# Kernel tuning notes

Measured on AMD Instinct MI355X. Metric: run time of the kernel, lower is better.

The kernel has to match this reference:

```python
import jax, jax.numpy as jnp
import numpy as np

DIM = 1024
NUM_HEADS = 16
HEAD_DIM = DIM // NUM_HEADS
MLP_DIM = 4 * DIM
EPS = 1e-5


def layer_norm(x, g, b):
    mu = jnp.mean(x, axis=-1, keepdims=True)
    var = jnp.mean(jnp.square(x - mu), axis=-1, keepdims=True)
    return (x - mu) * jax.lax.rsqrt(var + EPS) * g + b


def setup_inputs() -> dict:
    key = jax.random.key(0)
    ks = jax.random.split(key, 12)
    B, L = 2, 2048
    s = lambda n: 1.0 / np.sqrt(n)
    return {
        "x": jax.random.normal(ks[0], (B, L, DIM), jnp.float32),
        "attn_mask": jnp.tril(jnp.ones((L, L), jnp.int32))[None, None],  # [1,1,L,L]
        "w_qkv": jax.random.normal(ks[1], (DIM, 3 * DIM), jnp.float32) * s(DIM),
        "b_qkv": jnp.zeros((3 * DIM,), jnp.float32),
        "w_proj": jax.random.normal(ks[2], (DIM, DIM), jnp.float32) * s(DIM),
        "b_proj": jnp.zeros((DIM,), jnp.float32),
        "w_fc1": jax.random.normal(ks[3], (DIM, MLP_DIM), jnp.float32) * s(DIM),
        "b_fc1": jnp.zeros((MLP_DIM,), jnp.float32),
        "w_fc2": jax.random.normal(ks[4], (MLP_DIM, DIM), jnp.float32) * s(MLP_DIM),
        "b_fc2": jnp.zeros((DIM,), jnp.float32),
        "g1": jnp.ones((DIM,), jnp.float32),
        "beta1": jnp.zeros((DIM,), jnp.float32),
        "g2": jnp.ones((DIM,), jnp.float32),
        "beta2": jnp.zeros((DIM,), jnp.float32),
    }


def reference(x, attn_mask, w_qkv, b_qkv, w_proj, b_proj, w_fc1, b_fc1,
              w_fc2, b_fc2, g1, beta1, g2, beta2):
    B, L, D = x.shape
    scale = HEAD_DIM ** -0.5

    # --- attention branch (pre-norm) ---
    h = layer_norm(x, g1, beta1)
    qkv = h @ w_qkv + b_qkv                                  # [B,L,3D]
    qkv = qkv.reshape(B, L, 3, NUM_HEADS, HEAD_DIM)
    q = qkv[:, :, 0].transpose(0, 2, 1, 3)                   # [B,H,L,hd]
    k = qkv[:, :, 1].transpose(0, 2, 1, 3)
    v = qkv[:, :, 2].transpose(0, 2, 1, 3)
    attn = jnp.einsum('bhqd,bhkd->bhqk', q, k) * scale       # [B,H,L,L]
    attn = jnp.where(attn_mask == 0, -jnp.inf, attn)
    attn = jax.nn.softmax(attn, axis=-1)
    y = jnp.einsum('bhqk,bhkd->bhqd', attn, v)               # [B,H,L,hd]
    y = y.transpose(0, 2, 1, 3).reshape(B, L, D)
    y = y @ w_proj + b_proj
    x = x + y

    # --- MLP branch (pre-norm) ---
    h = layer_norm(x, g2, beta2)
    h = jax.nn.gelu(h @ w_fc1 + b_fc1, approximate=False)
    h = h @ w_fc2 + b_fc2
    return x + h
```

## Files before the change

### kernel.cpp

```cpp
#include <hip/hip_runtime.h>
#include <hip/hip_bf16.h>
#include <stdint.h>

typedef unsigned short u16;
typedef __attribute__((ext_vector_type(8))) short bf16x8;
typedef __attribute__((ext_vector_type(4))) float f32x4;
typedef __attribute__((ext_vector_type(4))) unsigned short u16x4;

#define DEVI static __device__ __forceinline__

DEVI u16 f2bf(float f) {
    unsigned int u = __builtin_bit_cast(unsigned int, f);
    return (u16)((u + 0x7fffu + ((u >> 16) & 1u)) >> 16);
}

DEVI float gelu_f(float v) {
    const float z = 1.5957691216f * (v + 0.044715f * v * v * v);
    return v / (1.0f + __expf(-z));
}

DEVI void async_copy16(const void* g, void* l) {
    __builtin_amdgcn_global_load_lds((const __attribute__((address_space(1))) void*)g,
                                     (__attribute__((address_space(3))) void*)l,
                                     16, 0, 0);
}

__global__ __launch_bounds__(256) void tcvt_kernel(const float* __restrict__ src,
                                                   u16* __restrict__ dst,
                                                   int K, int N) {
    __shared__ float tile[32][33];
    const int k0 = blockIdx.x * 32, n0 = blockIdx.y * 32;
    const int t = threadIdx.x;
    const int c = t & 31, r0 = t >> 5;
#pragma unroll
    for (int p = 0; p < 4; ++p) {
        const int r = r0 + p * 8;
        tile[r][c] = src[(size_t)(k0 + r) * N + n0 + c];
    }
    __syncthreads();
#pragma unroll
    for (int p = 0; p < 4; ++p) {
        const int r = r0 + p * 8;
        dst[(size_t)(n0 + r) * K + k0 + c] = f2bf(tile[c][r]);
    }
}

__global__ __launch_bounds__(256) void ln_kernel(const float* __restrict__ x,
                                                 const float* __restrict__ gw,
                                                 const float* __restrict__ bw,
                                                 u16* __restrict__ out) {
    const int row = blockIdx.x;
    const int t = threadIdx.x;
    const float4 v = ((const float4*)(x + (size_t)row * 1024))[t];
    float s  = v.x + v.y + v.z + v.w;
    float ss = v.x * v.x + v.y * v.y + v.z * v.z + v.w * v.w;
#pragma unroll
    for (int off = 32; off > 0; off >>= 1) {
        s  += __shfl_down(s, off);
        ss += __shfl_down(ss, off);
    }
    __shared__ float red[8];
    const int wv = t >> 6;
    if ((t & 63) == 0) { red[wv] = s; red[4 + wv] = ss; }
    __syncthreads();
    if (t == 0) {
        red[0] = red[0] + red[1] + red[2] + red[3];
        red[4] = red[4] + red[5] + red[6] + red[7];
    }
    __syncthreads();
    const float mean = red[0] * (1.0f / 1024.0f);
    const float var  = red[4] * (1.0f / 1024.0f) - mean * mean;
    const float rstd = rsqrtf(var + 1e-5f);
    const float4 gv = ((const float4*)gw)[t];
    const float4 bv = ((const float4*)bw)[t];
    u16x4 o;
    o[0] = f2bf((v.x - mean) * rstd * gv.x + bv.x);
    o[1] = f2bf((v.y - mean) * rstd * gv.y + bv.y);
    o[2] = f2bf((v.z - mean) * rstd * gv.z + bv.z);
    o[3] = f2bf((v.w - mean) * rstd * gv.w + bv.w);
    ((u16x4*)out)[(size_t)row * 256 + t] = o;
}

DEVI void stage64(const char* g, size_t ldb, char* lds0, int lane, int wv) {
    const int colsw = ((lane & 3) << 4) ^ (lane & 32);
    const int rl = lane >> 2;
#pragma unroll
    for (int i = 0; i < 4; ++i) {
        const int s = wv * 4 + i;
        const int kh = s >> 3, c = s & 7;
        async_copy16(g + (size_t)(c * 16 + rl) * ldb + kh * 64 + colsw,
                     lds0 + s * 1024);
    }
}

template <int EPI, int SPLITK>
__global__ __launch_bounds__(256, 4) void gemmv6(const u16* __restrict__ A,
                                                 const u16* __restrict__ Bt,
                                                 const float* __restrict__ bias,
                                                 void* __restrict__ out0,
                                                 void* __restrict__ out1,
                                                 void* __restrict__ out2,
                                                 int M, int N, int K) {
    __shared__ __align__(16) char As[16384];
    __shared__ __align__(16) char Bs[16384];
    const int tid = threadIdx.x;
    const int lane = tid & 63, wv = tid >> 6;
    const int wr = wv >> 1, wc = wv & 1;
    const int g = lane >> 4, qq = lane & 15;
    const int rdoff = qq * 64 + ((g * 16) ^ ((qq & 8) << 2));

    const int nwg = gridDim.x;
    int id = blockIdx.x;
    id = (id & 7) * (nwg >> 3) + (id >> 3);
    const int MT = M >> 7, NTn = N >> 7;
    const int slice = id / (MT * NTn);
    const int r2 = id % (MT * NTn);
    const int m0 = (r2 % MT) << 7;
    const int n0 = (r2 / MT) << 7;
    const int Ks = K / SPLITK;
    const int NT = Ks >> 6;
    const size_t ldb = (size_t)K * 2;

    const char* pa = (const char*)A + (size_t)m0 * ldb + (size_t)slice * Ks * 2;
    const char* pb = (const char*)Bt + (size_t)n0 * ldb + (size_t)slice * Ks * 2;

    f32x4 acc[4][4] = {};

    for (int t = 0; t < NT; ++t) {
        stage64(pa + (size_t)t * 128, ldb, As, lane, wv);
        stage64(pb + (size_t)t * 128, ldb, Bs, lane, wv);
        __syncthreads();
#pragma unroll
        for (int kh = 0; kh < 2; ++kh) {
            bf16x8 fa[4], fb[4];
#pragma unroll
            for (int fn = 0; fn < 4; ++fn)
                fb[fn] = *(const bf16x8*)(Bs + (kh * 8 + wc * 4 + fn) * 1024 + rdoff);
#pragma unroll
            for (int fm = 0; fm < 4; ++fm)
                fa[fm] = *(const bf16x8*)(As + (kh * 8 + wr * 4 + fm) * 1024 + rdoff);
#pragma unroll
            for (int fm = 0; fm < 4; ++fm)
#pragma unroll
                for (int fn = 0; fn < 4; ++fn)
                    acc[fm][fn] = __builtin_amdgcn_mfma_f32_16x16x32_bf16(fa[fm], fb[fn],
                                                                          acc[fm][fn], 0, 0, 0);
        }
        __syncthreads();
    }

#pragma unroll
    for (int fm = 0; fm < 4; ++fm) {
#pragma unroll
        for (int fn = 0; fn < 4; ++fn) {
            const int mrow = m0 + wr * 64 + fm * 16 + g * 4;
            const int ncol = n0 + wc * 64 + fn * 16 + qq;
            if constexpr (EPI == 0) {
                const float bs = bias[ncol];
                const int sec = ncol >> 10;
                const int hd_ = ncol & 1023;
                const int hh = hd_ >> 6, dd = hd_ & 63;
                if (sec == 2) {
                    const int b_ = mrow >> 11, l_ = mrow & 2047;
                    u16x4 pk;
#pragma unroll
                    for (int r = 0; r < 4; ++r) pk[r] = f2bf(acc[fm][fn][r] + bs);
                    *(u16x4*)((u16*)out2 + ((size_t)((b_ * 16 + hh) * 64 + dd)) * 2048 + l_) = pk;
                } else {
                    u16* dst = (sec == 0) ? (u16*)out0 : (u16*)out1;
                    const float sc = (sec == 0) ? 0.125f : 1.0f;
#pragma unroll
                    for (int r = 0; r < 4; ++r) {
                        const int mr = mrow + r;
                        const int b_ = mr >> 11, l_ = mr & 2047;
                        dst[((size_t)((b_ * 16 + hh) * 2048 + l_)) * 64 + dd] =
                            f2bf((acc[fm][fn][r] + bs) * sc);
                    }
                }
            } else if constexpr (EPI == 2) {
                const float bs = bias[ncol];
                u16* dst = (u16*)out0;
#pragma unroll
                for (int r = 0; r < 4; ++r)
                    dst[(size_t)(mrow + r) * N + ncol] = f2bf(gelu_f(acc[fm][fn][r] + bs));
            } else {
                float* dst = (float*)out0 + (size_t)slice * M * N;
#pragma unroll
                for (int r = 0; r < 4; ++r)
                    dst[(size_t)(mrow + r) * N + ncol] = acc[fm][fn][r];
            }
        }
    }
}

template <int SPLIT>
__global__ __launch_bounds__(256) void reduceN_kernel(const float* __restrict__ p,
                                                      const float* __restrict__ bias,
                                                      const float* __restrict__ res,
                                                      float* __restrict__ out,
                                                      int MN4, int N4) {
    const int i = blockIdx.x * 256 + threadIdx.x;
    float4 s = ((const float4*)p)[i];
#pragma unroll
    for (int s2 = 1; s2 < SPLIT; ++s2) {
        const float4 q = ((const float4*)p)[(size_t)s2 * MN4 + i];
        s.x += q.x; s.y += q.y; s.z += q.z; s.w += q.w;
    }
    const float4 r = ((const float4*)res)[i];
    const float4 bs = ((const float4*)bias)[i & (N4 - 1)];
    float4 o;
    o.x = s.x + r.x + bs.x;
    o.y = s.y + r.y + bs.y;
    o.z = s.z + r.z + bs.z;
    o.w = s.w + r.w + bs.w;
    ((float4*)out)[i] = o;
}

DEVI void stage_kv(const char* kbase, const char* vbase, int key0,
                   u16* ksm, u16* vsm, int wv, int lane) {
#pragma unroll
    for (int i = 0; i < 2; ++i) {
        const int c = wv + i * 4;
        const int off = c * 1024 + lane * 16;
        const int row = off >> 7;
        const int scol = (off & 127) ^ ((row & 7) << 4);
        async_copy16(kbase + (size_t)key0 * 128 + (size_t)row * 128 + scol,
                     (char*)ksm + c * 1024);
    }
#pragma unroll
    for (int i = 0; i < 2; ++i) {
        const int c = wv + i * 4;
        const int row = c * 8 + (lane >> 3);
        const int scol = ((lane & 7) * 16) ^ ((row & 7) << 4);
        async_copy16(vbase + (size_t)row * 4096 + (size_t)key0 * 2 + scol,
                     (char*)vsm + c * 1024);
    }
}

__global__ __launch_bounds__(256, 3) void attn_kernel(const u16* __restrict__ Q,
                                                      const u16* __restrict__ Kk,
                                                      const u16* __restrict__ Vt,
                                                      u16* __restrict__ Y) {
    const int bh = blockIdx.y;
    const int b_ = bh >> 4, hh = bh & 15;
    const int qb = gridDim.x - 1 - blockIdx.x;
    const int tid = threadIdx.x;
    const int wv = tid >> 6, lane = tid & 63;
    const int g = lane >> 4, qi = lane & 15;
    const int xsw = (qi & 7) << 4;
    const int q0 = qb * 64 + wv * 16;
    const int qg = q0 + qi;

    __shared__ __align__(16) u16 Ksm[2][4096];
    __shared__ __align__(16) u16 Vsm[2][4096];
    __shared__ __align__(16) u16 Pl[4][16][72];

    const u16*  Qb = Q + ((size_t)bh * 2048 + q0) * 64;
    const char* Kb = (const char*)(Kk + (size_t)bh * 2048 * 64);
    const char* Vb = (const char*)(Vt + (size_t)bh * 64 * 2048);

    bf16x8 qf[2];
#pragma unroll
    for (int ks = 0; ks < 2; ++ks)
        qf[ks] = *(const bf16x8*)(Qb + qi * 64 + ks * 32 + g * 8);

    f32x4 oacc[4] = {};
    float m_run = -1e30f, l_run = 0.0f;
    const int ntile = qb + 1;

    stage_kv(Kb, Vb, 0, Ksm[0], Vsm[0], wv, lane);
    __syncthreads();

    int cur = 0;
    for (int kt = 0; kt < ntile; ++kt) {
        const int key0 = kt * 64;
        if (kt + 1 < ntile)
            stage_kv(Kb, Vb, key0 + 64, Ksm[cur ^ 1], Vsm[cur ^ 1], wv, lane);

        f32x4 sacc[4] = {};
#pragma unroll
        for (int ks = 0; ks < 2; ++ks) {
#pragma unroll
            for (int kc = 0; kc < 4; ++kc) {
                const int rk = kc * 16 + qi;
                const bf16x8 ak = *(const bf16x8*)((const char*)Ksm[cur] + rk * 128 +
                                                   ((ks * 64 + g * 16) ^ xsw));
                sacc[kc] = __builtin_amdgcn_mfma_f32_16x16x32_bf16(ak, qf[ks], sacc[kc], 0, 0, 0);
            }
        }

        float p[4][4];
        float mymax = -1e30f;
        if (kt == ntile - 1) {
#pragma unroll
            for (int kc = 0; kc < 4; ++kc) {
#pragma unroll
                for (int r = 0; r < 4; ++r) {
                    const int key = key0 + kc * 16 + g * 4 + r;
                    float sv = sacc[kc][r];
                    if (key > qg) sv = -__builtin_inff();
                    p[kc][r] = sv;
                    mymax = fmaxf(mymax, sv);
                }
            }
        } else {
#pragma unroll
            for (int kc = 0; kc < 4; ++kc) {
#pragma unroll
                for (int r = 0; r < 4; ++r) {
                    p[kc][r] = sacc[kc][r];
                    mymax = fmaxf(mymax, sacc[kc][r]);
                }
            }
        }
        mymax = fmaxf(mymax, __shfl_xor(mymax, 16));
        mymax = fmaxf(mymax, __shfl_xor(mymax, 32));
        const float m_new = fmaxf(m_run, mymax);
        const float alpha = __expf(m_run - m_new);
        float lsum = 0.0f;
#pragma unroll
        for (int kc = 0; kc < 4; ++kc) {
#pragma unroll
            for (int r = 0; r < 4; ++r) {
                const float e = __expf(p[kc][r] - m_new);
                p[kc][r] = e;
                lsum += e;
            }
        }
        lsum += __shfl_xor(lsum, 16);
        lsum += __shfl_xor(lsum, 32);
        l_run = l_run * alpha + lsum;
        m_run = m_new;
#pragma unroll
        for (int c = 0; c < 4; ++c) {
#pragma unroll
            for (int r = 0; r < 4; ++r) oacc[c][r] *= alpha;
        }
#pragma unroll
        for (int kc = 0; kc < 4; ++kc) {
            u16x4 pk;
#pragma unroll
            for (int r = 0; r < 4; ++r) pk[r] = f2bf(p[kc][r]);
            *(u16x4*)(&Pl[wv][qi][kc * 16 + g * 4]) = pk;
        }
        bf16x8 pb[2];
#pragma unroll
        for (int ks = 0; ks < 2; ++ks)
            pb[ks] = *(const bf16x8*)(&Pl[wv][qi][ks * 32 + g * 8]);
#pragma unroll
        for (int ks = 0; ks < 2; ++ks) {
#pragma unroll
            for (int c = 0; c < 4; ++c) {
                const int rv = c * 16 + qi;
                const bf16x8 av = *(const bf16x8*)((const char*)Vsm[cur] + rv * 128 +
                                                   ((ks * 64 + g * 16) ^ xsw));
                oacc[c] = __builtin_amdgcn_mfma_f32_16x16x32_bf16(av, pb[ks], oacc[c], 0, 0, 0);
            }
        }
        __syncthreads();
        cur ^= 1;
    }

    const float inv = 1.0f / l_run;
#pragma unroll
    for (int c = 0; c < 4; ++c) {
        u16x4 o;
#pragma unroll
        for (int r = 0; r < 4; ++r) o[r] = f2bf(oacc[c][r] * inv);
        *(u16x4*)(&Y[((size_t)(b_ * 2048 + qg)) * 1024 + hh * 64 + c * 16 + g * 4]) = o;
    }
}

extern "C" void kernel_launch(void* const* d_in, const int* in_sizes, int n_in,
                              void* d_out, int out_size, void* d_ws, size_t ws_size,
                              hipStream_t stream) {
    (void)in_sizes; (void)n_in; (void)out_size;
    const float* x      = (const float*)d_in[0];
    const float* w_qkv  = (const float*)d_in[2];
    const float* b_qkv  = (const float*)d_in[3];
    const float* w_proj = (const float*)d_in[4];
    const float* b_proj = (const float*)d_in[5];
    const float* w_fc1  = (const float*)d_in[6];
    const float* b_fc1  = (const float*)d_in[7];
    const float* w_fc2  = (const float*)d_in[8];
    const float* b_fc2  = (const float*)d_in[9];
    const float* g1     = (const float*)d_in[10];
    const float* be1    = (const float*)d_in[11];
    const float* g2     = (const float*)d_in[12];
    const float* be2    = (const float*)d_in[13];

    char* ws = (char*)d_ws;
    size_t off = 0;
    auto alloc = [&](size_t bytes) { size_t r = off; off += (bytes + 255) & ~(size_t)255; return r; };
    u16*   wt_qkv = (u16*)(ws + alloc((size_t)3072 * 1024 * 2));
    u16*   wt_prj = (u16*)(ws + alloc((size_t)1024 * 1024 * 2));
    u16*   wt_fc1 = (u16*)(ws + alloc((size_t)4096 * 1024 * 2));
    u16*   wt_fc2 = (u16*)(ws + alloc((size_t)1024 * 4096 * 2));
    u16*   hbuf   = (u16*)(ws + alloc((size_t)4096 * 1024 * 2));
    float* x1     = (float*)(ws + alloc((size_t)4096 * 1024 * 4));
    char*  big    = ws + alloc((size_t)33554432);
    u16* qb  = (u16*)(big);
    u16* kb  = (u16*)(big + 8388608);
    u16* vtb = (u16*)(big + 16777216);
    u16* yb  = (u16*)(big + 25165824);
    u16* act = (u16*)(big);
    if (off > ws_size) return;
    const size_t part_need = (size_t)4 * 4096 * 1024 * 4;
    if ((ws_size - off) < part_need) return;
    float* part = (float*)(ws + off);

    const dim3 blk(256);
    tcvt_kernel<<<dim3(32, 96), blk, 0, stream>>>(w_qkv, wt_qkv, 1024, 3072);
    tcvt_kernel<<<dim3(32, 32), blk, 0, stream>>>(w_proj, wt_prj, 1024, 1024);
    tcvt_kernel<<<dim3(32, 128), blk, 0, stream>>>(w_fc1, wt_fc1, 1024, 4096);
    tcvt_kernel<<<dim3(128, 32), blk, 0, stream>>>(w_fc2, wt_fc2, 4096, 1024);

    ln_kernel<<<dim3(4096), blk, 0, stream>>>(x, g1, be1, hbuf);
    gemmv6<0, 1><<<dim3(768), blk, 0, stream>>>(hbuf, wt_qkv, b_qkv,
                                                qb, kb, vtb, 4096, 3072, 1024);
    attn_kernel<<<dim3(32, 32), blk, 0, stream>>>(qb, kb, vtb, yb);
    gemmv6<4, 2><<<dim3(512), blk, 0, stream>>>(yb, wt_prj, nullptr,
                                                part, nullptr, nullptr, 4096, 1024, 1024);
    reduceN_kernel<2><<<dim3(4096), blk, 0, stream>>>(part, b_proj, x, x1, 1048576, 256);
    ln_kernel<<<dim3(4096), blk, 0, stream>>>(x1, g2, be2, hbuf);
    gemmv6<2, 1><<<dim3(1024), blk, 0, stream>>>(hbuf, wt_fc1, b_fc1,
                                                 act, nullptr, nullptr, 4096, 4096, 1024);
    gemmv6<4, 4><<<dim3(1024), blk, 0, stream>>>(act, wt_fc2, nullptr,
                                                 part, nullptr, nullptr, 4096, 1024, 4096);
    reduceN_kernel<4><<<dim3(4096), blk, 0, stream>>>(part, b_fc2, x1, (float*)d_out,
                                                      1048576, 256);
}
```

Before: 270.5 us.

## Rewrite attention with 32x32 MFMA, 128-row query blocks, paired causal tiles

Replaces the 16x16 MFMA flash-attention kernel with one using 32x32x16 MFMA over 128-query blocks, where each workgroup handles two complementary query blocks to balance the causal workload. Q is pre-scaled by log2(e)/sqrt(d) so softmax can use exp2 directly. A lazy rescale only updates the running max when it grows by more than a threshold. The aim is fewer instructions per FLOP and better load balance, at the cost of a smaller grid (256 blocks) and more per-thread registers.

```diff
diff --git a/kernel.cpp b/kernel.cpp
--- a/kernel.cpp
+++ b/kernel.cpp
@@ -5,6 +5,7 @@
 typedef unsigned short u16;
 typedef __attribute__((ext_vector_type(8))) short bf16x8;
 typedef __attribute__((ext_vector_type(4))) float f32x4;
+typedef __attribute__((ext_vector_type(16))) float f32x16;
 typedef __attribute__((ext_vector_type(4))) unsigned short u16x4;
 
 #define DEVI static __device__ __forceinline__
@@ -168,7 +169,7 @@
                     *(u16x4*)((u16*)out2 + ((size_t)((b_ * 16 + hh) * 64 + dd)) * 2048 + l_) = pk;
                 } else {
                     u16* dst = (sec == 0) ? (u16*)out0 : (u16*)out1;
-                    const float sc = (sec == 0) ? 0.125f : 1.0f;
+                    const float sc = (sec == 0) ? 0.1803368801f : 1.0f;
 #pragma unroll
                     for (int r = 0; r < 4; ++r) {
                         const int mr = mrow + r;
@@ -237,137 +238,138 @@
     }
 }
 
-__global__ __launch_bounds__(256, 3) void attn_kernel(const u16* __restrict__ Q,
-                                                      const u16* __restrict__ Kk,
-                                                      const u16* __restrict__ Vt,
-                                                      u16* __restrict__ Y) {
+__global__ __launch_bounds__(256, 3) void attn32_kernel(const u16* __restrict__ Q,
+                                                        const u16* __restrict__ Kk,
+                                                        const u16* __restrict__ Vt,
+                                                        u16* __restrict__ Y) {
     const int bh = blockIdx.y;
     const int b_ = bh >> 4, hh = bh & 15;
-    const int qb = gridDim.x - 1 - blockIdx.x;
+    const int bx = blockIdx.x;
     const int tid = threadIdx.x;
     const int wv = tid >> 6, lane = tid & 63;
-    const int g = lane >> 4, qi = lane & 15;
-    const int xsw = (qi & 7) << 4;
-    const int q0 = qb * 64 + wv * 16;
-    const int qg = q0 + qi;
+    const int hi = lane >> 5, qc = lane & 31;
 
     __shared__ __align__(16) u16 Ksm[2][4096];
     __shared__ __align__(16) u16 Vsm[2][4096];
-    __shared__ __align__(16) u16 Pl[4][16][72];
-
-    const u16*  Qb = Q + ((size_t)bh * 2048 + q0) * 64;
+    __shared__ __align__(16) u16 Pl[4][32 * 72];
+
     const char* Kb = (const char*)(Kk + (size_t)bh * 2048 * 64);
     const char* Vb = (const char*)(Vt + (size_t)bh * 64 * 2048);
-
-    bf16x8 qf[2];
-#pragma unroll
-    for (int ks = 0; ks < 2; ++ks)
-        qf[ks] = *(const bf16x8*)(Qb + qi * 64 + ks * 32 + g * 8);
-
-    f32x4 oacc[4] = {};
-    float m_run = -1e30f, l_run = 0.0f;
-    const int ntile = qb + 1;
-
-    stage_kv(Kb, Vb, 0, Ksm[0], Vsm[0], wv, lane);
-    __syncthreads();
-
-    int cur = 0;
-    for (int kt = 0; kt < ntile; ++kt) {
-        const int key0 = kt * 64;
-        if (kt + 1 < ntile)
-            stage_kv(Kb, Vb, key0 + 64, Ksm[cur ^ 1], Vsm[cur ^ 1], wv, lane);
-
-        f32x4 sacc[4] = {};
-#pragma unroll
-        for (int ks = 0; ks < 2; ++ks) {
-#pragma unroll
-            for (int kc = 0; kc < 4; ++kc) {
-                const int rk = kc * 16 + qi;
-                const bf16x8 ak = *(const bf16x8*)((const char*)Ksm[cur] + rk * 128 +
-                                                   ((ks * 64 + g * 16) ^ xsw));
-                sacc[kc] = __builtin_amdgcn_mfma_f32_16x16x32_bf16(ak, qf[ks], sacc[kc], 0, 0, 0);
-            }
+    u16* Pw = &Pl[wv][0];
+    const u16* Pr = Pw + qc * 72;
+
+#pragma unroll 1
+    for (int part = 0; part < 2; ++part) {
+        const int qb = part ? bx : (15 - bx);
+        const int q0w = qb * 128 + wv * 32;
+        const int qg = q0w + qc;
+        const int ntile = qb * 2 + 2;
+        const int ntile_w = qb * 2 + (wv >> 1) + 1;
+
+        bf16x8 qf[4];
+        {
+            const u16* Qp = Q + ((size_t)bh * 2048 + q0w + qc) * 64;
+#pragma unroll
+            for (int c = 0; c < 4; ++c)
+                qf[c] = *(const bf16x8*)(Qp + c * 16 + hi * 8);
         }
 
-        float p[4][4];
-        float mymax = -1e30f;
-        if (kt == ntile - 1) {
-#pragma unroll
-            for (int kc = 0; kc < 4; ++kc) {
-#pragma unroll
-                for (int r = 0; r < 4; ++r) {
-                    const int key = key0 + kc * 16 + g * 4 + r;
-                    float sv = sacc[kc][r];
-                    if (key > qg) sv = -__builtin_inff();
-                    p[kc][r] = sv;
-                    mymax = fmaxf(mymax, sv);
+        f32x16 oacc[2];
+#pragma unroll
+        for (int r = 0; r < 16; ++r) { oacc[0][r] = 0.0f; oacc[1][r] = 0.0f; }
+        float m_run = -1e30f, l_run = 0.0f;
+
+        stage_kv(Kb, Vb, 0, Ksm[0], Vsm[0], wv, lane);
+        __syncthreads();
+        int cur = 0;
+        for (int kt = 0; kt < ntile; ++kt) {
+            const int key0 = kt * 64;
+            if (kt + 1 < ntile)
+                stage_kv(Kb, Vb, key0 + 64, Ksm[cur ^ 1], Vsm[cur ^ 1], wv, lane);
+            if (kt < ntile_w) {
+                f32x16 sacc[2];
+#pragma unroll
+                for (int r = 0; r < 16; ++r) { sacc[0][r] = 0.0f; sacc[1][r] = 0.0f; }
+#pragma unroll
+                for (int c = 0; c < 4; ++c) {
+#pragma unroll
+                    for (int kb = 0; kb < 2; ++kb) {
+                        const int kr = kb * 32 + qc;
+                        const bf16x8 ak = *(const bf16x8*)((const char*)Ksm[cur] + kr * 128 +
+                                              ((c * 32 + hi * 16) ^ ((kr & 7) << 4)));
+                        sacc[kb] = __builtin_amdgcn_mfma_f32_32x32x16_bf16(ak, qf[c],
+                                                                           sacc[kb], 0, 0, 0);
+                    }
+                }
+                float pmax = -1e30f;
+                if (key0 + 63 > q0w) {
+#pragma unroll
+                    for (int kb = 0; kb < 2; ++kb)
+#pragma unroll
+                        for (int r = 0; r < 16; ++r) {
+                            const int key = key0 + kb * 32 + (r & 3) + 8 * (r >> 2) + 4 * hi;
+                            float s = sacc[kb][r];
+                            if (key > qg) s = -1e30f;
+                            sacc[kb][r] = s;
+                            pmax = fmaxf(pmax, s);
+                        }
+                } else {
+#pragma unroll
+                    for (int kb = 0; kb < 2; ++kb)
+#pragma unroll
+                        for (int r = 0; r < 16; ++r) pmax = fmaxf(pmax, sacc[kb][r]);
+                }
+                pmax = fmaxf(pmax, __shfl_xor(pmax, 32));
+                if (pmax > m_run + 11.0f) {
+                    const float alpha = __builtin_amdgcn_exp2f(m_run - pmax);
+#pragma unroll
+                    for (int r = 0; r < 16; ++r) { oacc[0][r] *= alpha; oacc[1][r] *= alpha; }
+                    l_run *= alpha;
+                    m_run = pmax;
+                }
+                float lsum = 0.0f;
+#pragma unroll
+                for (int kb = 0; kb < 2; ++kb)
+#pragma unroll
+                    for (int j = 0; j < 4; ++j) {
+                        u16x4 pk4;
+#pragma unroll
+                        for (int t = 0; t < 4; ++t) {
+                            const float e = __builtin_amdgcn_exp2f(sacc[kb][j * 4 + t] - m_run);
+                            lsum += e;
+                            pk4[t] = f2bf(e);
+                        }
+                        *(u16x4*)(Pw + qc * 72 + kb * 32 + j * 8 + 4 * hi) = pk4;
+                    }
+                lsum += __shfl_xor(lsum, 32);
+                l_run += lsum;
+#pragma unroll
+                for (int c = 0; c < 4; ++c) {
+                    const bf16x8 pf = *(const bf16x8*)(Pr + c * 16 + hi * 8);
+#pragma unroll
+                    for (int db = 0; db < 2; ++db) {
+                        const int dr = db * 32 + qc;
+                        const bf16x8 av = *(const bf16x8*)((const char*)Vsm[cur] + dr * 128 +
+                                              ((c * 32 + hi * 16) ^ ((dr & 7) << 4)));
+                        oacc[db] = __builtin_amdgcn_mfma_f32_32x32x16_bf16(av, pf,
+                                                                           oacc[db], 0, 0, 0);
+                    }
                 }
             }
-        } else {
-#pragma unroll
-            for (int kc = 0; kc < 4; ++kc) {
-#pragma unroll
-                for (int r = 0; r < 4; ++r) {
-                    p[kc][r] = sacc[kc][r];
-                    mymax = fmaxf(mymax, sacc[kc][r]);
-                }
+            __syncthreads();
+            cur ^= 1;
+        }
+        const float inv = 1.0f / l_run;
+        u16* Yp = &Y[((size_t)(b_ * 2048 + qg)) * 1024 + hh * 64];
+#pragma unroll
+        for (int db = 0; db < 2; ++db)
+#pragma unroll
+            for (int j = 0; j < 4; ++j) {
+                u16x4 o;
+#pragma unroll
+                for (int t = 0; t < 4; ++t) o[t] = f2bf(oacc[db][j * 4 + t] * inv);
+                *(u16x4*)(Yp + db * 32 + j * 8 + 4 * hi) = o;
             }
-        }
-        mymax = fmaxf(mymax, __shfl_xor(mymax, 16));
-        mymax = fmaxf(mymax, __shfl_xor(mymax, 32));
-        const float m_new = fmaxf(m_run, mymax);
-        const float alpha = __expf(m_run - m_new);
-        float lsum = 0.0f;
-#pragma unroll
-        for (int kc = 0; kc < 4; ++kc) {
-#pragma unroll
-            for (int r = 0; r < 4; ++r) {
-                const float e = __expf(p[kc][r] - m_new);
-                p[kc][r] = e;
-                lsum += e;
-            }
-        }
-        lsum += __shfl_xor(lsum, 16);
-        lsum += __shfl_xor(lsum, 32);
-        l_run = l_run * alpha + lsum;
-        m_run = m_new;
-#pragma unroll
-        for (int c = 0; c < 4; ++c) {
-#pragma unroll
-            for (int r = 0; r < 4; ++r) oacc[c][r] *= alpha;
-        }
-#pragma unroll
-        for (int kc = 0; kc < 4; ++kc) {
-            u16x4 pk;
-#pragma unroll
-            for (int r = 0; r < 4; ++r) pk[r] = f2bf(p[kc][r]);
-            *(u16x4*)(&Pl[wv][qi][kc * 16 + g * 4]) = pk;
-        }
-        bf16x8 pb[2];
-#pragma unroll
-        for (int ks = 0; ks < 2; ++ks)
-            pb[ks] = *(const bf16x8*)(&Pl[wv][qi][ks * 32 + g * 8]);
-#pragma unroll
-        for (int ks = 0; ks < 2; ++ks) {
-#pragma unroll
-            for (int c = 0; c < 4; ++c) {
-                const int rv = c * 16 + qi;
-                const bf16x8 av = *(const bf16x8*)((const char*)Vsm[cur] + rv * 128 +
-                                                   ((ks * 64 + g * 16) ^ xsw));
-                oacc[c] = __builtin_amdgcn_mfma_f32_16x16x32_bf16(av, pb[ks], oacc[c], 0, 0, 0);
-            }
-        }
-        __syncthreads();
-        cur ^= 1;
-    }
-
-    const float inv = 1.0f / l_run;
-#pragma unroll
-    for (int c = 0; c < 4; ++c) {
-        u16x4 o;
-#pragma unroll
-        for (int r = 0; r < 4; ++r) o[r] = f2bf(oacc[c][r] * inv);
-        *(u16x4*)(&Y[((size_t)(b_ * 2048 + qg)) * 1024 + hh * 64 + c * 16 + g * 4]) = o;
     }
 }
 
@@ -418,7 +420,7 @@
     ln_kernel<<<dim3(4096), blk, 0, stream>>>(x, g1, be1, hbuf);
     gemmv6<0, 1><<<dim3(768), blk, 0, stream>>>(hbuf, wt_qkv, b_qkv,
                                                 qb, kb, vtb, 4096, 3072, 1024);
-    attn_kernel<<<dim3(32, 32), blk, 0, stream>>>(qb, kb, vtb, yb);
+    attn32_kernel<<<dim3(8, 32), blk, 0, stream>>>(qb, kb, vtb, yb);
     gemmv6<4, 2><<<dim3(512), blk, 0, stream>>>(yb, wt_prj, nullptr,
                                                 part, nullptr, nullptr, 4096, 1024, 1024);
     reduceN_kernel<2><<<dim3(4096), blk, 0, stream>>>(part, b_proj, x, x1, 1048576, 256);
```

Result: faster. 249.5 us (-7.8%).
